# Kernel tuning notes

Measured on AMD Instinct MI355X. Metric: run time of the kernel, lower is better.

Reference implementation:

```python
import jax, jax.numpy as jnp
import numpy as np
import itertools

RANKS_HIGH = 15
SUITS_HIGH = 5
B, M = 16, 24
# Omaha unspool: choose 2 of 4 hole cards x choose 3 of 5 board cards -> 60 five-card combos
COMBOS = np.array([h + b for h in itertools.combinations(range(4), 2)
                   for b in itertools.combinations(range(4, 9), 3)], dtype=np.int32)  # [60, 5]


def setup_inputs() -> dict:
    key = jax.random.key(0)
    ks = list(jax.random.split(key, 20))
    f = lambda i, shape: jax.random.normal(ks[i], shape, jnp.float32) * 0.05
    ranks = jax.random.randint(ks[0], (B, M, 9), 2, RANKS_HIGH)  # card ranks 2..14
    suits = jax.random.randint(ks[1], (B, M, 9), 1, SUITS_HIGH)  # suits 1..4
    x = jnp.stack([ranks, suits], axis=-1).reshape(B, M, 18)     # alternating rank/suit
    ones16 = jnp.ones((16,), jnp.float32)
    zeros16 = jnp.zeros((16,), jnp.float32)
    return {
        "x": x,
        "suit_w": f(2, (16, 5, 1)), "suit_b": f(3, (16,)),
        "rank_w": f(4, (16, 5, 5)), "rank_b": f(5, (16,)),
        "bn_s_gamma": ones16, "bn_s_beta": zeros16, "bn_s_mean": zeros16, "bn_s_var": ones16,
        "bn_r_gamma": ones16, "bn_r_beta": zeros16, "bn_r_mean": zeros16, "bn_r_var": ones16,
        "w1": f(6, (32, 16)), "b1": f(7, (32,)),
        "w2": f(8, (32, 32)), "b2": f(9, (32,)),
        "wc": f(10, (7463, 512)), "bc": f(11, (7463,)),
        "wo1": f(12, (512, 15360)), "bo1": f(13, (512,)),
        "wo2": f(14, (256, 512)), "bo2": f(15, (256,)),
        "wo3": f(16, (127, 256)), "bo3": f(17, (127,)),
    }


def _bn(t, gamma, beta, mean, var, eps=1e-5):
    # eval-mode BatchNorm1d; channel axis is -2 (shape [..., 16, L])
    inv = gamma / jnp.sqrt(var + eps)
    return t * inv[:, None] + (beta - mean * inv)[:, None]


def _forward(x, suit_w, suit_b, bn_s_gamma, bn_s_beta, bn_s_mean, bn_s_var,
             rank_w, rank_b, bn_r_gamma, bn_r_beta, bn_r_mean, bn_r_var,
             w1, b1, w2, b2, wc, bc, wo1, bo1, wo2, bo2, wo3, bo3):
    b, m, _ = x.shape
    ranks = x[..., 0::2][..., COMBOS]  # [B,M,60,5]
    suits = x[..., 1::2][..., COMBOS]  # [B,M,60,5]
    hot_r = jax.nn.one_hot(ranks, RANKS_HIGH, dtype=jnp.float32)  # [B,M,60,5,15]
    hot_s = jax.nn.one_hot(suits, SUITS_HIGH, dtype=jnp.float32)  # [B,M,60,5,5]
    # suit conv: Conv1d(5,16,k=1) over the one-hot length; channels = 5 cards
    s = jnp.einsum('bmkcl,oc->bmkol', hot_s, suit_w[:, :, 0]) + suit_b[:, None]
    s = jax.nn.relu(_bn(s, bn_s_gamma, bn_s_beta, bn_s_mean, bn_s_var))  # [B,M,60,16,5]
    # rank conv: Conv1d(5,16,k=5) valid: length 15 -> 11
    n = b * m * 60
    r = jax.lax.conv_general_dilated(hot_r.reshape(n, 5, RANKS_HIGH), rank_w,
                                     window_strides=(1,), padding='VALID',
                                     dimension_numbers=('NCH', 'OIH', 'NCH'))
    r = r.reshape(b, m, 60, 16, 11) + rank_b[:, None]
    r = jax.nn.relu(_bn(r, bn_r_gamma, bn_r_beta, bn_r_mean, bn_r_var))  # [B,M,60,16,11]
    raw = jnp.concatenate([r, s], axis=-1)  # [B,M,60,16,16]
    # hand-class head: two hidden linears on last dim, then 512 -> 7463
    h = jax.nn.relu(raw @ w1.T + b1)        # [B,M,60,16,32]
    h = jax.nn.relu(h @ w2.T + b2)          # [B,M,60,16,32]
    logits = h.reshape(b, m, 60, 512) @ wc.T + bc  # [B,M,60,7463]
    best = jnp.min(jnp.argmax(jax.lax.stop_gradient(logits), axis=-1),
                   axis=-1, keepdims=True)  # [B,M,1] (lower class index = better hand)
    # raw-feature head: [B,M,60*16*16=15360] -> 512 -> 256 -> 127
    o = raw.reshape(b, m, 60 * 16 * 16)
    o = jax.nn.relu(o @ wo1.T + bo1)
    o = jax.nn.relu(o @ wo2.T + bo2)
    o = jax.nn.relu(o @ wo3.T + bo3)
    return jnp.concatenate([o, best.astype(o.dtype)], axis=-1)  # [B,M,128]


def reference(x, suit_w, suit_b, bn_s_gamma, bn_s_beta, bn_s_mean, bn_s_var,
              rank_w, rank_b, bn_r_gamma, bn_r_beta, bn_r_mean, bn_r_var,
              w1, b1, w2, b2, wc, bc, wo1, bo1, wo2, bo2, wo3, bo3):
    return _forward(x, suit_w, suit_b, bn_s_gamma, bn_s_beta, bn_s_mean, bn_s_var,
                    rank_w, rank_b, bn_r_gamma, bn_r_beta, bn_r_mean, bn_r_var,
                    w1, b1, w2, b2, wc, bc, wo1, bo1, wo2, bo2, wo3, bo3)
```

## Files before the change

kernel.cpp:

```cpp
#include <hip/hip_runtime.h>

#define NSAMP 384
#define NCOMBO 60
#define NROW 23040
#define KDIM 512
#define NCLS 7463
#define NCLSP 7680
#define NTILE_N 30
#define NTILE_M 180
#define O1_NZ 30
#define O1_KZ 512

typedef short s16x8 __attribute__((ext_vector_type(8)));
typedef short s16x4 __attribute__((ext_vector_type(4)));
typedef float f32x4 __attribute__((ext_vector_type(4)));

__device__ unsigned short g_wc_hi[NCLSP * KDIM];
__device__ unsigned short g_wc_lo[NCLSP * KDIM];
__device__ unsigned short g_h_hi[NROW * KDIM];
__device__ unsigned short g_h_lo[NROW * KDIM];
__device__ unsigned short g_rawbf[NROW * 256];
__device__ unsigned short g_wo1bf[512 * 15360];
__device__ float          g_pmax[NTILE_N * NROW];
__device__ int            g_pidx[NTILE_N * NROW];
__device__ float          g_part[O1_NZ * NSAMP * 512];

__device__ __forceinline__ float bf2f(unsigned short u){
  union { unsigned int i; float f; } v; v.i = ((unsigned int)u) << 16; return v.f;
}
__device__ __forceinline__ unsigned short f2bf(float f){
  union { float f; unsigned int i; } v; v.f = f;
  unsigned int u = v.i;
  unsigned int r = (u + 0x7FFFu + ((u >> 16) & 1u)) >> 16;
  return (unsigned short)r;
}
__device__ __forceinline__ void gload16(const void* g, void* l){
  __builtin_amdgcn_global_load_lds((const __attribute__((address_space(1))) void*)g,
                                   (__attribute__((address_space(3))) void*)l, 16, 0, 0);
}

__global__ __launch_bounds__(256) void k_prep(const float* __restrict__ wc,
                                              const float* __restrict__ wo1)
{
  int b = blockIdx.x;
  if (b < 3840){
    int idx = (b * 256 + threadIdx.x) * 4;
    float4 w = {0.f, 0.f, 0.f, 0.f};
    if (idx < NCLS * KDIM) w = *(const float4*)(wc + idx);
    s16x4 hi, lo;
    float wv[4] = {w.x, w.y, w.z, w.w};
    #pragma unroll
    for (int i = 0; i < 4; ++i){
      unsigned short h = f2bf(wv[i]);
      hi[i] = (short)h;
      lo[i] = (short)f2bf(wv[i] - bf2f(h));
    }
    *(s16x4*)(g_wc_hi + idx) = hi;
    *(s16x4*)(g_wc_lo + idx) = lo;
  } else {
    int idx = ((b - 3840) * 256 + threadIdx.x) * 4;
    float4 w = *(const float4*)(wo1 + idx);
    s16x4 v;
    v[0] = (short)f2bf(w.x); v[1] = (short)f2bf(w.y);
    v[2] = (short)f2bf(w.z); v[3] = (short)f2bf(w.w);
    *(s16x4*)(g_wo1bf + idx) = v;
  }
}

__global__ __launch_bounds__(256) void k_features(
    const int* __restrict__ x,
    const float* __restrict__ suit_w, const float* __restrict__ suit_b,
    const float* __restrict__ rank_w, const float* __restrict__ rank_b,
    const float* __restrict__ bns_g, const float* __restrict__ bns_b,
    const float* __restrict__ bns_m, const float* __restrict__ bns_v,
    const float* __restrict__ bnr_g, const float* __restrict__ bnr_b,
    const float* __restrict__ bnr_m, const float* __restrict__ bnr_v,
    const float* __restrict__ w1, const float* __restrict__ b1,
    const float* __restrict__ w2, const float* __restrict__ b2)
{
  __shared__ float raw_s[4][256];
  __shared__ float h1_s[4][512];
  const int tid  = threadIdx.x;
  const int lane = tid & 63;
  const int wv   = tid >> 6;
  const int combo = blockIdx.x * 4 + wv;
  const int s = combo / 60;
  const int k = combo % 60;
  const int hp = k / 10, bt = k % 10;
  const int HP0[6]  = {0,0,0,1,1,2}, HP1[6] = {1,2,3,2,3,3};
  const int BT0[10] = {4,4,4,4,4,4,5,5,5,6};
  const int BT1[10] = {5,5,5,6,6,7,6,6,7,7};
  const int BT2[10] = {6,7,8,7,8,8,7,8,8,8};
  int cards[5] = {HP0[hp], HP1[hp], BT0[bt], BT1[bt], BT2[bt]};
  const int* xp = x + s * 18;
  int rk[5], st[5];
  #pragma unroll
  for (int c = 0; c < 5; ++c){ rk[c] = xp[2*cards[c]]; st[c] = xp[2*cards[c] + 1]; }

  {
    s16x4 rv;
    #pragma unroll
    for (int i = 0; i < 4; ++i){
      int e = lane * 4 + i;
      int o = e >> 4, l = e & 15;
      float v;
      if (l < 11){
        float a = 0.f;
        #pragma unroll
        for (int c = 0; c < 5; ++c){
          int d = rk[c] - l;
          if (d >= 0 && d < 5) a += rank_w[o*25 + c*5 + d];
        }
        a += rank_b[o];
        float inv = bnr_g[o] / sqrtf(bnr_v[o] + 1e-5f);
        v = a * inv + (bnr_b[o] - bnr_m[o] * inv);
      } else {
        int j = l - 11;
        float a = suit_b[o];
        #pragma unroll
        for (int c = 0; c < 5; ++c) if (st[c] == j) a += suit_w[o*5 + c];
        float inv = bns_g[o] / sqrtf(bns_v[o] + 1e-5f);
        v = a * inv + (bns_b[o] - bns_m[o] * inv);
      }
      v = fmaxf(v, 0.f);
      raw_s[wv][e] = v;
      rv[i] = (short)f2bf(v);
    }
    *(s16x4*)(g_rawbf + (size_t)s * 15360 + k * 256 + lane * 4) = rv;
  }
  __syncthreads();
  #pragma unroll
  for (int i = 0; i < 8; ++i){
    int e = lane + 64 * i;
    int o = e >> 5, j = e & 31;
    float a = b1[j];
    #pragma unroll
    for (int l = 0; l < 16; ++l) a += raw_s[wv][o*16 + l] * w1[j*16 + l];
    h1_s[wv][e] = fmaxf(a, 0.f);
  }
  __syncthreads();
  {
    s16x8 hv, lv;
    #pragma unroll
    for (int i = 0; i < 8; ++i){
      int e = lane * 8 + i;
      int o = e >> 5, j = e & 31;
      float a = b2[j];
      #pragma unroll
      for (int l = 0; l < 32; ++l) a += h1_s[wv][o*32 + l] * w2[j*32 + l];
      a = fmaxf(a, 0.f);
      unsigned short h = f2bf(a);
      hv[i] = (short)h;
      lv[i] = (short)f2bf(a - bf2f(h));
    }
    *(s16x8*)(g_h_hi + (size_t)combo * 512 + lane * 8) = hv;
    *(s16x8*)(g_h_lo + (size_t)combo * 512 + lane * 8) = lv;
  }
}

__global__ __launch_bounds__(512, 4) void k_logits(const float* __restrict__ bc)
{
  __shared__ unsigned char lds[49152];
  const int tid  = threadIdx.x;
  const int lane = tid & 63;
  const int wv   = tid >> 6;
  const int wm   = wv >> 2, wn = wv & 3;
  const int blk  = blockIdx.x;
  const int nt   = blk / NTILE_M;
  const int mt   = blk % NTILE_M;
  const int m0 = mt * 128;
  const int n0 = nt * 256;

  f32x4 acc[4][4];
  #pragma unroll
  for (int i = 0; i < 4; ++i)
    #pragma unroll
    for (int j = 0; j < 4; ++j)
      acc[i][j] = (f32x4){0.f, 0.f, 0.f, 0.f};

  const int rS = wv * 16 + (lane >> 2);
  const int cS = (lane & 3) ^ ((lane >> 3) & 3);
  auto stage = [&](int buf, int t){
    const int p = t / 3, seg = t - p * 3;
    const int kc = p * 32;
    const unsigned short* As = (seg < 2) ? g_h_hi : g_h_lo;
    const unsigned short* Bs = (seg == 1) ? g_wc_lo : g_wc_hi;
    const unsigned base = buf * 24576 + wv * 1024;
    gload16(As + (size_t)(m0 + rS) * KDIM + kc + cS * 8, lds + base);
    gload16(Bs + (size_t)(n0 + rS) * KDIM + kc + cS * 8, lds + base + 8192);
    gload16(Bs + (size_t)(n0 + 128 + rS) * KDIM + kc + cS * 8, lds + base + 16384);
  };

  stage(0, 0);
  stage(1, 1);
  asm volatile("s_waitcnt vmcnt(3)" ::: "memory");
  __builtin_amdgcn_sched_barrier(0);
  __builtin_amdgcn_s_barrier();
  asm volatile("" ::: "memory");

  const int q = lane >> 4;
  #pragma unroll 1
  for (int t = 0; t < 48; ++t){
    const unsigned cb = (unsigned)(t & 1) * 24576;
    s16x8 af[4], bf[4];
    #pragma unroll
    for (int i = 0; i < 4; ++i){
      int row = wm * 64 + i * 16 + (lane & 15);
      af[i] = *(const s16x8*)(lds + cb + row * 64 + ((q ^ ((row >> 1) & 3)) << 4));
    }
    #pragma unroll
    for (int j = 0; j < 4; ++j){
      int row = wn * 64 + j * 16 + (lane & 15);
      bf[j] = *(const s16x8*)(lds + cb + 8192 + row * 64 + ((q ^ ((row >> 1) & 3)) << 4));
    }
    __builtin_amdgcn_s_setprio(1);
    #pragma unroll
    for (int i = 0; i < 4; ++i)
      #pragma unroll
      for (int j = 0; j < 4; ++j)
        acc[i][j] = __builtin_amdgcn_mfma_f32_16x16x32_bf16(af[i], bf[j], acc[i][j], 0, 0, 0);
    __builtin_amdgcn_s_setprio(0);
    __builtin_amdgcn_sched_barrier(0);
    __builtin_amdgcn_s_barrier();
    asm volatile("" ::: "memory");
    if (t + 2 < 48){
      stage(t & 1, t + 2);
      asm volatile("s_waitcnt vmcnt(3)" ::: "memory");
    } else {
      asm volatile("s_waitcnt vmcnt(0)" ::: "memory");
    }
    __builtin_amdgcn_sched_barrier(0);
    __builtin_amdgcn_s_barrier();
    asm volatile("" ::: "memory");
  }

  float* cmax = (float*)lds;
  int*   cidx = (int*)(lds + 2048);
  const int g = lane >> 4;
  #pragma unroll
  for (int i = 0; i < 4; ++i){
    #pragma unroll
    for (int r = 0; r < 4; ++r){
      float bv = -__builtin_inff(); int bi = 0x7FFFFFFF;
      #pragma unroll
      for (int j = 0; j < 4; ++j){
        int col = n0 + wn * 64 + j * 16 + (lane & 15);
        if (col < NCLS){
          float v = acc[i][j][r] + bc[col];
          if (v > bv){ bv = v; bi = col; }
        }
      }
      for (int s = 1; s < 16; s <<= 1){
        float ov = __shfl_xor(bv, s);
        int   oi = __shfl_xor(bi, s);
        if (ov > bv || (ov == bv && oi < bi)){ bv = ov; bi = oi; }
      }
      if ((lane & 15) == 0){
        int rloc = wm * 64 + i * 16 + g * 4 + r;
        cmax[rloc * 4 + wn] = bv;
        cidx[rloc * 4 + wn] = bi;
      }
    }
  }
  __syncthreads();
  if (tid < 128){
    float bv = cmax[tid * 4]; int bi = cidx[tid * 4];
    #pragma unroll
    for (int wq = 1; wq < 4; ++wq){
      float v = cmax[tid * 4 + wq]; int i1 = cidx[tid * 4 + wq];
      if (v > bv || (v == bv && i1 < bi)){ bv = v; bi = i1; }
    }
    size_t row = (size_t)(m0 + tid);
    g_pmax[(size_t)nt * NROW + row] = bv;
    g_pidx[(size_t)nt * NROW + row] = bi;
  }
}

__global__ __launch_bounds__(256) void k_o1(void)
{
  __shared__ unsigned char As[16384];
  __shared__ unsigned char Bs[16384];
  const int tid  = threadIdx.x;
  const int lane = tid & 63;
  const int wv   = tid >> 6;
  const int wr   = wv >> 1, wq = wv & 1;
  const int n0  = blockIdx.x * 128;
  const int m0  = blockIdx.y * 128;
  const int kc0 = blockIdx.z * O1_KZ;

  f32x4 acc[4][4];
  #pragma unroll
  for (int i = 0; i < 4; ++i)
    #pragma unroll
    for (int j = 0; j < 4; ++j)
      acc[i][j] = (f32x4){0.f, 0.f, 0.f, 0.f};

  const int rA = lane >> 3;
  const int c0 = lane & 7;
  for (int kk = 0; kk < O1_KZ; kk += 64){
    int kc = kc0 + kk;
    __syncthreads();
    #pragma unroll
    for (int it = 0; it < 4; ++it){
      int seg = wv * 4 + it;
      int r   = seg * 8 + rA;
      int cs  = c0 ^ (r & 7);
      gload16(g_rawbf + (size_t)(m0 + r) * 15360 + kc + cs * 8, As + seg * 1024);
      gload16(g_wo1bf + (size_t)(n0 + r) * 15360 + kc + cs * 8, Bs + seg * 1024);
    }
    __syncthreads();
    #pragma unroll
    for (int ks = 0; ks < 2; ++ks){
      int q = ks * 4 + (lane >> 4);
      s16x8 a[4];
      #pragma unroll
      for (int i = 0; i < 4; ++i){
        int row = wr * 64 + i * 16 + (lane & 15);
        a[i] = *(const s16x8*)(As + row * 128 + ((q ^ (row & 7)) * 16));
      }
      #pragma unroll
      for (int j = 0; j < 4; ++j){
        int col = wq * 64 + j * 16 + (lane & 15);
        s16x8 b = *(const s16x8*)(Bs + col * 128 + ((q ^ (col & 7)) * 16));
        #pragma unroll
        for (int i = 0; i < 4; ++i)
          acc[i][j] = __builtin_amdgcn_mfma_f32_16x16x32_bf16(a[i], b, acc[i][j], 0, 0, 0);
      }
    }
  }
  const int g = lane >> 4;
  #pragma unroll
  for (int i = 0; i < 4; ++i)
    #pragma unroll
    for (int j = 0; j < 4; ++j)
      #pragma unroll
      for (int r = 0; r < 4; ++r){
        int gm = m0 + wr * 64 + i * 16 + g * 4 + r;
        int gn = n0 + wq * 64 + j * 16 + (lane & 15);
        g_part[((size_t)blockIdx.z * NSAMP + gm) * 512 + gn] = acc[i][j][r];
      }
}

__global__ __launch_bounds__(256) void k_tail(
    const float* __restrict__ bo1, const float* __restrict__ wo2,
    const float* __restrict__ bo2, const float* __restrict__ wo3,
    const float* __restrict__ bo3, float* __restrict__ out)
{
  __shared__ float o1f[512];
  __shared__ float o2f[256];
  __shared__ int   bis[60];
  const int s = blockIdx.x;
  const int tid = threadIdx.x;
  if (tid < 60){
    size_t row = (size_t)s * 60 + tid;
    float bv = -__builtin_inff(); int bi = 0x7FFFFFFF;
    for (int qn = 0; qn < NTILE_N; ++qn){
      float v = g_pmax[(size_t)qn * NROW + row];
      int   i = g_pidx[(size_t)qn * NROW + row];
      if (v > bv || (v == bv && i < bi)){ bv = v; bi = i; }
    }
    bis[tid] = bi;
  }
  for (int j = tid; j < 512; j += 256){
    float a = bo1[j];
    for (int ks = 0; ks < O1_NZ; ++ks) a += g_part[((size_t)ks * NSAMP + s) * 512 + j];
    o1f[j] = fmaxf(a, 0.f);
  }
  __syncthreads();
  {
    float a = bo2[tid];
    const float* wr = wo2 + (size_t)tid * 512;
    for (int i = 0; i < 512; i += 4){
      float4 w4 = *(const float4*)(wr + i);
      a += o1f[i]*w4.x + o1f[i+1]*w4.y + o1f[i+2]*w4.z + o1f[i+3]*w4.w;
    }
    o2f[tid] = fmaxf(a, 0.f);
  }
  __syncthreads();
  if (tid < 127){
    float a = bo3[tid];
    const float* wr = wo3 + (size_t)tid * 256;
    for (int i = 0; i < 256; i += 4){
      float4 w4 = *(const float4*)(wr + i);
      a += o2f[i]*w4.x + o2f[i+1]*w4.y + o2f[i+2]*w4.z + o2f[i+3]*w4.w;
    }
    out[s * 128 + tid] = fmaxf(a, 0.f);
  }
  if (tid == 0){
    int m = bis[0];
    for (int i = 1; i < 60; ++i) m = min(m, bis[i]);
    out[s * 128 + 127] = (float)m;
  }
}

extern "C" void kernel_launch(void* const* d_in, const int* in_sizes, int n_in,
                              void* d_out, int out_size, void* d_ws, size_t ws_size,
                              hipStream_t stream)
{
  (void)d_ws; (void)ws_size; (void)in_sizes; (void)n_in; (void)out_size;
  const int*   x      = (const int*)  d_in[0];
  const float* suit_w = (const float*)d_in[1];
  const float* suit_b = (const float*)d_in[2];
  const float* rank_w = (const float*)d_in[3];
  const float* rank_b = (const float*)d_in[4];
  const float* bns_g  = (const float*)d_in[5];
  const float* bns_b  = (const float*)d_in[6];
  const float* bns_m  = (const float*)d_in[7];
  const float* bns_v  = (const float*)d_in[8];
  const float* bnr_g  = (const float*)d_in[9];
  const float* bnr_b  = (const float*)d_in[10];
  const float* bnr_m  = (const float*)d_in[11];
  const float* bnr_v  = (const float*)d_in[12];
  const float* w1     = (const float*)d_in[13];
  const float* b1     = (const float*)d_in[14];
  const float* w2     = (const float*)d_in[15];
  const float* b2     = (const float*)d_in[16];
  const float* wc     = (const float*)d_in[17];
  const float* bc     = (const float*)d_in[18];
  const float* wo1    = (const float*)d_in[19];
  const float* bo1    = (const float*)d_in[20];
  const float* wo2    = (const float*)d_in[21];
  const float* bo2    = (const float*)d_in[22];
  const float* wo3    = (const float*)d_in[23];
  const float* bo3    = (const float*)d_in[24];
  float* out = (float*)d_out;

  hipLaunchKernelGGL(k_prep, dim3(11520), dim3(256), 0, stream, wc, wo1);
  hipLaunchKernelGGL(k_features, dim3(5760), dim3(256), 0, stream, x,
                     suit_w, suit_b, rank_w, rank_b,
                     bns_g, bns_b, bns_m, bns_v, bnr_g, bnr_b, bnr_m, bnr_v,
                     w1, b1, w2, b2);
  hipLaunchKernelGGL(k_logits, dim3(NTILE_N * NTILE_M), dim3(512), 0, stream, bc);
  hipLaunchKernelGGL(k_o1, dim3(4, 3, O1_NZ), dim3(256), 0, stream);
  hipLaunchKernelGGL(k_tail, dim3(NSAMP), dim3(256), 0, stream,
                     bo1, wo2, bo2, wo3, bo3, out);
}
```

Measured before the change: 1.083 ms.

## Double the logits GEMM M tile and deepen to a four-stage LDS pipeline

The k_logits GEMM block tile grows from 128x256 to 256x256, so each warp accumulates 8x4 MFMA tiles and reuses its B fragments across two A halves. Global-to-LDS staging becomes a 4-buffer ring that prefetches three k-steps ahead, in 128KB of dynamic shared memory. The LDS layout drops the XOR swizzle for a chunk-major 16-row layout, and the argmax epilogue is widened to 256 rows. The aim is to cut the global traffic of re-reading Wc per M tile and to hide load latency better. The cost is one block per CU, higher register pressure, and possible LDS bank conflicts or a launch failure if the large dynamic LDS request is not allowed.

After: 1.158 ms. 1.07x slower.

```diff
diff --git a/kernel.cpp b/kernel.cpp
--- a/kernel.cpp
+++ b/kernel.cpp
@@ -7,7 +7,7 @@
 #define NCLS 7463
 #define NCLSP 7680
 #define NTILE_N 30
-#define NTILE_M 180
+#define NTILE_M 90
 #define O1_NZ 30
 #define O1_KZ 512
 
@@ -158,9 +158,9 @@
   }
 }
 
-__global__ __launch_bounds__(512, 4) void k_logits(const float* __restrict__ bc)
-{
-  __shared__ unsigned char lds[49152];
+__global__ __launch_bounds__(512, 2) void k_logits(const float* __restrict__ bc)
+{
+  extern __shared__ unsigned char lds[];
   const int tid  = threadIdx.x;
   const int lane = tid & 63;
   const int wv   = tid >> 6;
@@ -168,77 +168,87 @@
   const int blk  = blockIdx.x;
   const int nt   = blk / NTILE_M;
   const int mt   = blk % NTILE_M;
-  const int m0 = mt * 128;
+  const int m0 = mt * 256;
   const int n0 = nt * 256;
 
-  f32x4 acc[4][4];
-  #pragma unroll
-  for (int i = 0; i < 4; ++i)
+  f32x4 acc[8][4];
+  #pragma unroll
+  for (int i = 0; i < 8; ++i)
     #pragma unroll
     for (int j = 0; j < 4; ++j)
       acc[i][j] = (f32x4){0.f, 0.f, 0.f, 0.f};
 
-  const int rS = wv * 16 + (lane >> 2);
-  const int cS = (lane & 3) ^ ((lane >> 3) & 3);
-  auto stage = [&](int buf, int t){
-    const int p = t / 3, seg = t - p * 3;
+  const int srow = lane & 15;
+  const int schk = lane >> 4;
+
+  auto stage_one = [&](int t, int it){
+    const int p = t / 3, seg3 = t - p * 3;
     const int kc = p * 32;
-    const unsigned short* As = (seg < 2) ? g_h_hi : g_h_lo;
-    const unsigned short* Bs = (seg == 1) ? g_wc_lo : g_wc_hi;
-    const unsigned base = buf * 24576 + wv * 1024;
-    gload16(As + (size_t)(m0 + rS) * KDIM + kc + cS * 8, lds + base);
-    gload16(Bs + (size_t)(n0 + rS) * KDIM + kc + cS * 8, lds + base + 8192);
-    gload16(Bs + (size_t)(n0 + 128 + rS) * KDIM + kc + cS * 8, lds + base + 16384);
+    const unsigned short* As = (seg3 < 2) ? g_h_hi : g_h_lo;
+    const unsigned short* Bs = (seg3 == 1) ? g_wc_lo : g_wc_hi;
+    const int sg = it * 8 + wv;
+    const unsigned db = ((unsigned)(t & 3)) * 32768 + sg * 1024;
+    gload16(As + (size_t)(m0 + sg * 16 + srow) * KDIM + kc + schk * 8, lds + db);
+    gload16(Bs + (size_t)(n0 + sg * 16 + srow) * KDIM + kc + schk * 8, lds + db + 16384);
   };
 
-  stage(0, 0);
-  stage(1, 1);
-  asm volatile("s_waitcnt vmcnt(3)" ::: "memory");
+  #pragma unroll
+  for (int t = 0; t < 3; ++t){ stage_one(t, 0); stage_one(t, 1); }
+  asm volatile("s_waitcnt vmcnt(8)" ::: "memory");
   __builtin_amdgcn_sched_barrier(0);
   __builtin_amdgcn_s_barrier();
-  asm volatile("" ::: "memory");
-
-  const int q = lane >> 4;
+
+  const int rr = lane & 15;
+  const int qq = lane >> 4;
+  s16x8 af[4], bfr[4];
   #pragma unroll 1
   for (int t = 0; t < 48; ++t){
-    const unsigned cb = (unsigned)(t & 1) * 24576;
-    s16x8 af[4], bf[4];
-    #pragma unroll
-    for (int i = 0; i < 4; ++i){
-      int row = wm * 64 + i * 16 + (lane & 15);
-      af[i] = *(const s16x8*)(lds + cb + row * 64 + ((q ^ ((row >> 1) & 3)) << 4));
-    }
-    #pragma unroll
-    for (int j = 0; j < 4; ++j){
-      int row = wn * 64 + j * 16 + (lane & 15);
-      bf[j] = *(const s16x8*)(lds + cb + 8192 + row * 64 + ((q ^ ((row >> 1) & 3)) << 4));
-    }
+    const unsigned cb = ((unsigned)(t & 3)) * 32768;
+    const unsigned ab = cb + wm * 8192 + qq * 256 + rr * 16;
+    const unsigned bb = cb + 16384 + wn * 4096 + qq * 256 + rr * 16;
+    #pragma unroll
+    for (int j = 0; j < 4; ++j) bfr[j] = *(const s16x8*)(lds + bb + j * 1024);
+    #pragma unroll
+    for (int i = 0; i < 4; ++i) af[i] = *(const s16x8*)(lds + ab + i * 1024);
+    if (t < 45) stage_one(t + 3, 0);
+    __builtin_amdgcn_s_barrier();
+    asm volatile("s_waitcnt lgkmcnt(0)" ::: "memory");
+    __builtin_amdgcn_sched_barrier(0);
     __builtin_amdgcn_s_setprio(1);
     #pragma unroll
     for (int i = 0; i < 4; ++i)
       #pragma unroll
       for (int j = 0; j < 4; ++j)
-        acc[i][j] = __builtin_amdgcn_mfma_f32_16x16x32_bf16(af[i], bf[j], acc[i][j], 0, 0, 0);
+        acc[i][j] = __builtin_amdgcn_mfma_f32_16x16x32_bf16(af[i], bfr[j], acc[i][j], 0, 0, 0);
     __builtin_amdgcn_s_setprio(0);
     __builtin_amdgcn_sched_barrier(0);
     __builtin_amdgcn_s_barrier();
-    asm volatile("" ::: "memory");
-    if (t + 2 < 48){
-      stage(t & 1, t + 2);
-      asm volatile("s_waitcnt vmcnt(3)" ::: "memory");
-    } else {
-      asm volatile("s_waitcnt vmcnt(0)" ::: "memory");
-    }
+    #pragma unroll
+    for (int i = 0; i < 4; ++i) af[i] = *(const s16x8*)(lds + ab + (4 + i) * 1024);
+    if (t < 45) stage_one(t + 3, 1);
+    __builtin_amdgcn_s_barrier();
+    asm volatile("s_waitcnt lgkmcnt(0)" ::: "memory");
+    __builtin_amdgcn_sched_barrier(0);
+    __builtin_amdgcn_s_setprio(1);
+    #pragma unroll
+    for (int i = 0; i < 4; ++i)
+      #pragma unroll
+      for (int j = 0; j < 4; ++j)
+        acc[4 + i][j] = __builtin_amdgcn_mfma_f32_16x16x32_bf16(af[i], bfr[j], acc[4 + i][j], 0, 0, 0);
+    __builtin_amdgcn_s_setprio(0);
+    __builtin_amdgcn_sched_barrier(0);
+    if (t < 45)       asm volatile("s_waitcnt vmcnt(8)" ::: "memory");
+    else if (t == 45) asm volatile("s_waitcnt vmcnt(4)" ::: "memory");
+    else if (t == 46) asm volatile("s_waitcnt vmcnt(0)" ::: "memory");
     __builtin_amdgcn_sched_barrier(0);
     __builtin_amdgcn_s_barrier();
-    asm volatile("" ::: "memory");
   }
 
   float* cmax = (float*)lds;
-  int*   cidx = (int*)(lds + 2048);
+  int*   cidx = (int*)(lds + 4096);
   const int g = lane >> 4;
   #pragma unroll
-  for (int i = 0; i < 4; ++i){
+  for (int i = 0; i < 8; ++i){
     #pragma unroll
     for (int r = 0; r < 4; ++r){
       float bv = -__builtin_inff(); int bi = 0x7FFFFFFF;
@@ -256,14 +266,14 @@
         if (ov > bv || (ov == bv && oi < bi)){ bv = ov; bi = oi; }
       }
       if ((lane & 15) == 0){
-        int rloc = wm * 64 + i * 16 + g * 4 + r;
+        int rloc = wm * 128 + i * 16 + g * 4 + r;
         cmax[rloc * 4 + wn] = bv;
         cidx[rloc * 4 + wn] = bi;
       }
     }
   }
   __syncthreads();
-  if (tid < 128){
+  if (tid < 256){
     float bv = cmax[tid * 4]; int bi = cidx[tid * 4];
     #pragma unroll
     for (int wq = 1; wq < 4; ++wq){
@@ -430,7 +440,7 @@
                      suit_w, suit_b, rank_w, rank_b,
                      bns_g, bns_b, bns_m, bns_v, bnr_g, bnr_b, bnr_m, bnr_v,
                      w1, b1, w2, b2);
-  hipLaunchKernelGGL(k_logits, dim3(NTILE_N * NTILE_M), dim3(512), 0, stream, bc);
+  hipLaunchKernelGGL(k_logits, dim3(NTILE_N * NTILE_M), dim3(512), 131072, stream, bc);
   hipLaunchKernelGGL(k_o1, dim3(4, 3, O1_NZ), dim3(256), 0, stream);
   hipLaunchKernelGGL(k_tail, dim3(NSAMP), dim3(256), 0, stream,
                      bo1, wo2, bo2, wo3, bo3, out);
```

## Retile logits GEMM to 256x64 blocks with A fragments streamed from global

Applied to the files above, without the earlier changes.

The hand-class logits GEMM moves from 128x256 tiles with 512 threads to 256x64 tiles with 256 threads. Each wave now loads its A (hidden-activation) MFMA fragments straight from global memory into registers, double-buffered across k-steps, and only the small B (weight) slice goes through a double-buffered LDS buffer. The per-block argmax no longer needs a cross-wave LDS reduction, because each wave owns the full 64-column slice of its rows. In exchange there are four times as many column tiles, so the A operand is re-read from L2 far more often, and the partial-argmax buffer and its downstream reduction grow to 120 tiles per row.

After: 1.652 ms. 52.6% more time.

```diff
diff --git a/kernel.cpp b/kernel.cpp
--- a/kernel.cpp
+++ b/kernel.cpp
@@ -6,8 +6,8 @@
 #define KDIM 512
 #define NCLS 7463
 #define NCLSP 7680
-#define NTILE_N 30
-#define NTILE_M 180
+#define NTILE_N 120
+#define NTILE_M 90
 #define O1_NZ 30
 #define O1_KZ 512
 
@@ -158,18 +158,19 @@
   }
 }
 
-__global__ __launch_bounds__(512, 4) void k_logits(const float* __restrict__ bc)
-{
-  __shared__ unsigned char lds[49152];
+__global__ __launch_bounds__(256, 3) void k_logits(const float* __restrict__ bc)
+{
+  __shared__ unsigned char Blds[10240];
   const int tid  = threadIdx.x;
   const int lane = tid & 63;
   const int wv   = tid >> 6;
-  const int wm   = wv >> 2, wn = wv & 3;
+  const int cc   = lane & 15;
+  const int qq   = lane >> 4;
   const int blk  = blockIdx.x;
-  const int nt   = blk / NTILE_M;
-  const int mt   = blk % NTILE_M;
-  const int m0 = mt * 128;
-  const int n0 = nt * 256;
+  const int mt   = blk / NTILE_N;
+  const int nt   = blk % NTILE_N;
+  const int m0 = mt * 256;
+  const int n0 = nt * 64;
 
   f32x4 acc[4][4];
   #pragma unroll
@@ -178,65 +179,68 @@
     for (int j = 0; j < 4; ++j)
       acc[i][j] = (f32x4){0.f, 0.f, 0.f, 0.f};
 
-  const int rS = wv * 16 + (lane >> 2);
-  const int cS = (lane & 3) ^ ((lane >> 3) & 3);
-  auto stage = [&](int buf, int t){
-    const int p = t / 3, seg = t - p * 3;
-    const int kc = p * 32;
-    const unsigned short* As = (seg < 2) ? g_h_hi : g_h_lo;
-    const unsigned short* Bs = (seg == 1) ? g_wc_lo : g_wc_hi;
-    const unsigned base = buf * 24576 + wv * 1024;
-    gload16(As + (size_t)(m0 + rS) * KDIM + kc + cS * 8, lds + base);
-    gload16(Bs + (size_t)(n0 + rS) * KDIM + kc + cS * 8, lds + base + 8192);
-    gload16(Bs + (size_t)(n0 + 128 + rS) * KDIM + kc + cS * 8, lds + base + 16384);
-  };
-
-  stage(0, 0);
-  stage(1, 1);
-  asm volatile("s_waitcnt vmcnt(3)" ::: "memory");
-  __builtin_amdgcn_sched_barrier(0);
-  __builtin_amdgcn_s_barrier();
-  asm volatile("" ::: "memory");
-
-  const int q = lane >> 4;
-  #pragma unroll 1
-  for (int t = 0; t < 48; ++t){
-    const unsigned cb = (unsigned)(t & 1) * 24576;
-    s16x8 af[4], bf[4];
-    #pragma unroll
-    for (int i = 0; i < 4; ++i){
-      int row = wm * 64 + i * 16 + (lane & 15);
-      af[i] = *(const s16x8*)(lds + cb + row * 64 + ((q ^ ((row >> 1) & 3)) << 4));
-    }
-    #pragma unroll
-    for (int j = 0; j < 4; ++j){
-      int row = wn * 64 + j * 16 + (lane & 15);
-      bf[j] = *(const s16x8*)(lds + cb + 8192 + row * 64 + ((q ^ ((row >> 1) & 3)) << 4));
-    }
+  const int arow = m0 + wv * 64 + cc;
+  const int bcol = n0 + wv * 16 + cc;
+  const unsigned bwoff = (wv * 16 + cc) * 80 + qq * 16;
+
+  s16x8 aA[4], aB[4];
+  s16x8 brA, brB;
+  s16x8 bFr[4];
+
+  {
+    brA = *(const s16x8*)(g_wc_hi + (size_t)bcol * KDIM + 0 + qq * 8);
+    brB = *(const s16x8*)(g_wc_lo + (size_t)bcol * KDIM + 0 + qq * 8);
+    #pragma unroll
+    for (int i = 0; i < 4; ++i)
+      aA[i] = *(const s16x8*)(g_h_hi + (size_t)(arow + i * 16) * KDIM + 0 + qq * 8);
+    asm volatile("s_waitcnt vmcnt(5)" ::: "memory");
+    *(s16x8*)(Blds + bwoff) = brA;
+    asm volatile("s_waitcnt lgkmcnt(0)" ::: "memory");
+    __builtin_amdgcn_sched_barrier(0);
+    __builtin_amdgcn_s_barrier();
+  }
+
+  auto tile_body = [&](s16x8 (&CUR)[4], s16x8 (&NXT)[4], s16x8& brC, s16x8& brN, int t){
+    const unsigned bb = (unsigned)(t & 1) * 5120;
+    #pragma unroll
+    for (int j = 0; j < 4; ++j)
+      bFr[j] = *(const s16x8*)(Blds + bb + (j * 16 + cc) * 80 + qq * 16);
+    if (t + 2 < 48){
+      int t2 = t + 2, p2 = t2 / 3, sg2 = t2 - p2 * 3;
+      const unsigned short* Bg = (sg2 == 1) ? g_wc_lo : g_wc_hi;
+      brN = *(const s16x8*)(Bg + (size_t)bcol * KDIM + p2 * 32 + qq * 8);
+    }
+    if (t + 1 < 48){
+      int t1 = t + 1, p1 = t1 / 3, sg1 = t1 - p1 * 3;
+      const unsigned short* Ag = (sg1 < 2) ? g_h_hi : g_h_lo;
+      #pragma unroll
+      for (int i = 0; i < 4; ++i)
+        NXT[i] = *(const s16x8*)(Ag + (size_t)(arow + i * 16) * KDIM + p1 * 32 + qq * 8);
+    }
+    if (t < 46)       asm volatile("s_waitcnt vmcnt(5)" ::: "memory");
+    else if (t == 46) asm volatile("s_waitcnt vmcnt(4)" ::: "memory");
+    else              asm volatile("s_waitcnt vmcnt(0)" ::: "memory");
+    if (t + 1 < 48)
+      *(s16x8*)(Blds + (unsigned)((t + 1) & 1) * 5120 + bwoff) = brC;
+    asm volatile("s_waitcnt lgkmcnt(0)" ::: "memory");
+    __builtin_amdgcn_sched_barrier(0);
     __builtin_amdgcn_s_setprio(1);
     #pragma unroll
     for (int i = 0; i < 4; ++i)
       #pragma unroll
       for (int j = 0; j < 4; ++j)
-        acc[i][j] = __builtin_amdgcn_mfma_f32_16x16x32_bf16(af[i], bf[j], acc[i][j], 0, 0, 0);
+        acc[i][j] = __builtin_amdgcn_mfma_f32_16x16x32_bf16(CUR[i], bFr[j], acc[i][j], 0, 0, 0);
     __builtin_amdgcn_s_setprio(0);
     __builtin_amdgcn_sched_barrier(0);
     __builtin_amdgcn_s_barrier();
-    asm volatile("" ::: "memory");
-    if (t + 2 < 48){
-      stage(t & 1, t + 2);
-      asm volatile("s_waitcnt vmcnt(3)" ::: "memory");
-    } else {
-      asm volatile("s_waitcnt vmcnt(0)" ::: "memory");
-    }
-    __builtin_amdgcn_sched_barrier(0);
-    __builtin_amdgcn_s_barrier();
-    asm volatile("" ::: "memory");
-  }
-
-  float* cmax = (float*)lds;
-  int*   cidx = (int*)(lds + 2048);
-  const int g = lane >> 4;
+  };
+
+  #pragma unroll 1
+  for (int tp = 0; tp < 24; ++tp){
+    tile_body(aA, aB, brB, brA, tp * 2);
+    tile_body(aB, aA, brA, brB, tp * 2 + 1);
+  }
+
   #pragma unroll
   for (int i = 0; i < 4; ++i){
     #pragma unroll
@@ -244,7 +248,7 @@
       float bv = -__builtin_inff(); int bi = 0x7FFFFFFF;
       #pragma unroll
       for (int j = 0; j < 4; ++j){
-        int col = n0 + wn * 64 + j * 16 + (lane & 15);
+        int col = n0 + j * 16 + cc;
         if (col < NCLS){
           float v = acc[i][j][r] + bc[col];
           if (v > bv){ bv = v; bi = col; }
@@ -255,24 +259,13 @@
         int   oi = __shfl_xor(bi, s);
         if (ov > bv || (ov == bv && oi < bi)){ bv = ov; bi = oi; }
       }
-      if ((lane & 15) == 0){
-        int rloc = wm * 64 + i * 16 + g * 4 + r;
-        cmax[rloc * 4 + wn] = bv;
-        cidx[rloc * 4 + wn] = bi;
-      }
-    }
-  }
-  __syncthreads();
-  if (tid < 128){
-    float bv = cmax[tid * 4]; int bi = cidx[tid * 4];
-    #pragma unroll
-    for (int wq = 1; wq < 4; ++wq){
-      float v = cmax[tid * 4 + wq]; int i1 = cidx[tid * 4 + wq];
-      if (v > bv || (v == bv && i1 < bi)){ bv = v; bi = i1; }
-    }
-    size_t row = (size_t)(m0 + tid);
-    g_pmax[(size_t)nt * NROW + row] = bv;
-    g_pidx[(size_t)nt * NROW + row] = bi;
+      if (cc == 0){
+        int rloc = wv * 64 + i * 16 + qq * 4 + r;
+        size_t row = (size_t)(m0 + rloc);
+        g_pmax[(size_t)nt * NROW + row] = bv;
+        g_pidx[(size_t)nt * NROW + row] = bi;
+      }
+    }
   }
 }
 
@@ -430,7 +423,7 @@
                      suit_w, suit_b, rank_w, rank_b,
                      bns_g, bns_b, bns_m, bns_v, bnr_g, bnr_b, bnr_m, bnr_v,
                      w1, b1, w2, b2);
-  hipLaunchKernelGGL(k_logits, dim3(NTILE_N * NTILE_M), dim3(512), 0, stream, bc);
+  hipLaunchKernelGGL(k_logits, dim3(NTILE_M * NTILE_N), dim3(256), 0, stream, bc);
   hipLaunchKernelGGL(k_o1, dim3(4, 3, O1_NZ), dim3(256), 0, stream);
   hipLaunchKernelGGL(k_tail, dim3(NSAMP), dim3(256), 0, stream,
                      bo1, wo2, bo2, wo3, bo3, out);
```

## Replace split-bf16 logits GEMM with fp16 GEMM plus top-2 exact rescoring

Applied to the files above, without the earlier changes.

Drops the three-pass hi/lo bf16 split for the 23040x7463x512 logits GEMM and uses a single fp16 MFMA pass, cutting MFMA work and operand traffic to about a third. To keep the argmax exact, each tile now keeps a top-2 candidate list. When the winner's margin is small, the tail kernel rescored near-tie candidates in double precision from fp32 weights and fp32 activations. The GEMM is also retiled to 128x128 tiles with 256 threads, a 64-wide K step, and an XCD-aware block mapping. In exchange it stores an extra fp32 copy of the activations and has a rare serial rescoring path in k_tail.

Measured after the change: 2.366 ms. 2.19x slower.

```diff
diff --git a/kernel.cpp b/kernel.cpp
--- a/kernel.cpp
+++ b/kernel.cpp
@@ -6,7 +6,7 @@
 #define KDIM 512
 #define NCLS 7463
 #define NCLSP 7680
-#define NTILE_N 30
+#define NTILE_N 60
 #define NTILE_M 180
 #define O1_NZ 30
 #define O1_KZ 512
@@ -14,15 +14,17 @@
 typedef short s16x8 __attribute__((ext_vector_type(8)));
 typedef short s16x4 __attribute__((ext_vector_type(4)));
 typedef float f32x4 __attribute__((ext_vector_type(4)));
-
-__device__ unsigned short g_wc_hi[NCLSP * KDIM];
-__device__ unsigned short g_wc_lo[NCLSP * KDIM];
-__device__ unsigned short g_h_hi[NROW * KDIM];
-__device__ unsigned short g_h_lo[NROW * KDIM];
+typedef _Float16 f16x8 __attribute__((ext_vector_type(8)));
+
+__device__ unsigned short g_wc_f16[NCLSP * KDIM];
+__device__ unsigned short g_h_f16[NROW * KDIM];
+__device__ float          g_h_f32[NROW * KDIM];
 __device__ unsigned short g_rawbf[NROW * 256];
 __device__ unsigned short g_wo1bf[512 * 15360];
-__device__ float          g_pmax[NTILE_N * NROW];
-__device__ int            g_pidx[NTILE_N * NROW];
+__device__ float          g_p1v[NTILE_N * NROW];
+__device__ int            g_p1i[NTILE_N * NROW];
+__device__ float          g_p2v[NTILE_N * NROW];
+__device__ int            g_p2i[NTILE_N * NROW];
 __device__ float          g_part[O1_NZ * NSAMP * 512];
 
 __device__ __forceinline__ float bf2f(unsigned short u){
@@ -34,9 +36,17 @@
   unsigned int r = (u + 0x7FFFu + ((u >> 16) & 1u)) >> 16;
   return (unsigned short)r;
 }
+__device__ __forceinline__ unsigned short f2h(float f){
+  union { _Float16 h; unsigned short s; } cv; cv.h = (_Float16)f; return cv.s;
+}
 __device__ __forceinline__ void gload16(const void* g, void* l){
   __builtin_amdgcn_global_load_lds((const __attribute__((address_space(1))) void*)g,
                                    (__attribute__((address_space(3))) void*)l, 16, 0, 0);
+}
+__device__ __forceinline__ void top2_merge(float& v1, int& i1, float& v2, int& i2,
+                                           float wv, int wi){
+  if (wv > v1 || (wv == v1 && wi < i1)){ v2 = v1; i2 = i1; v1 = wv; i1 = wi; }
+  else if (wv > v2 || (wv == v2 && wi < i2)){ v2 = wv; i2 = wi; }
 }
 
 __global__ __launch_bounds__(256) void k_prep(const float* __restrict__ wc,
@@ -47,16 +57,9 @@
     int idx = (b * 256 + threadIdx.x) * 4;
     float4 w = {0.f, 0.f, 0.f, 0.f};
     if (idx < NCLS * KDIM) w = *(const float4*)(wc + idx);
-    s16x4 hi, lo;
-    float wv[4] = {w.x, w.y, w.z, w.w};
-    #pragma unroll
-    for (int i = 0; i < 4; ++i){
-      unsigned short h = f2bf(wv[i]);
-      hi[i] = (short)h;
-      lo[i] = (short)f2bf(wv[i] - bf2f(h));
-    }
-    *(s16x4*)(g_wc_hi + idx) = hi;
-    *(s16x4*)(g_wc_lo + idx) = lo;
+    ushort4 h;
+    h.x = f2h(w.x); h.y = f2h(w.y); h.z = f2h(w.z); h.w = f2h(w.w);
+    *(ushort4*)(g_wc_f16 + idx) = h;
   } else {
     int idx = ((b - 3840) * 256 + threadIdx.x) * 4;
     float4 w = *(const float4*)(wo1 + idx);
@@ -140,7 +143,8 @@
   }
   __syncthreads();
   {
-    s16x8 hv, lv;
+    unsigned short hv[8];
+    float hf[8];
     #pragma unroll
     for (int i = 0; i < 8; ++i){
       int e = lane * 8 + i;
@@ -149,27 +153,32 @@
       #pragma unroll
       for (int l = 0; l < 32; ++l) a += h1_s[wv][o*32 + l] * w2[j*32 + l];
       a = fmaxf(a, 0.f);
-      unsigned short h = f2bf(a);
-      hv[i] = (short)h;
-      lv[i] = (short)f2bf(a - bf2f(h));
-    }
-    *(s16x8*)(g_h_hi + (size_t)combo * 512 + lane * 8) = hv;
-    *(s16x8*)(g_h_lo + (size_t)combo * 512 + lane * 8) = lv;
-  }
-}
-
-__global__ __launch_bounds__(512, 4) void k_logits(const float* __restrict__ bc)
-{
-  __shared__ unsigned char lds[49152];
+      hv[i] = f2h(a);
+      hf[i] = a;
+    }
+    *(ushort4*)(g_h_f16 + (size_t)combo * 512 + lane * 8)     = *(ushort4*)&hv[0];
+    *(ushort4*)(g_h_f16 + (size_t)combo * 512 + lane * 8 + 4) = *(ushort4*)&hv[4];
+    *(float4*)(g_h_f32 + (size_t)combo * 512 + lane * 8)     = *(float4*)&hf[0];
+    *(float4*)(g_h_f32 + (size_t)combo * 512 + lane * 8 + 4) = *(float4*)&hf[4];
+  }
+}
+
+__global__ __launch_bounds__(256, 2) void k_logits(const float* __restrict__ bc)
+{
+  __shared__ unsigned char lds[65536];
   const int tid  = threadIdx.x;
   const int lane = tid & 63;
   const int wv   = tid >> 6;
-  const int wm   = wv >> 2, wn = wv & 3;
-  const int blk  = blockIdx.x;
-  const int nt   = blk / NTILE_M;
-  const int mt   = blk % NTILE_M;
+  const int wr   = wv >> 1, wq = wv & 1;
+  const int flat  = blockIdx.x;
+  const int xcd   = flat & 7;
+  const int seq   = flat >> 3;
+  const int group = xcd >> 1;
+  const int par   = xcd & 1;
+  const int mt    = (seq / 15) * 2 + par;
+  const int nt    = group * 15 + (seq % 15);
   const int m0 = mt * 128;
-  const int n0 = nt * 256;
+  const int n0 = nt * 128;
 
   f32x4 acc[4][4];
   #pragma unroll
@@ -178,101 +187,92 @@
     for (int j = 0; j < 4; ++j)
       acc[i][j] = (f32x4){0.f, 0.f, 0.f, 0.f};
 
-  const int rS = wv * 16 + (lane >> 2);
-  const int cS = (lane & 3) ^ ((lane >> 3) & 3);
-  auto stage = [&](int buf, int t){
-    const int p = t / 3, seg = t - p * 3;
-    const int kc = p * 32;
-    const unsigned short* As = (seg < 2) ? g_h_hi : g_h_lo;
-    const unsigned short* Bs = (seg == 1) ? g_wc_lo : g_wc_hi;
-    const unsigned base = buf * 24576 + wv * 1024;
-    gload16(As + (size_t)(m0 + rS) * KDIM + kc + cS * 8, lds + base);
-    gload16(Bs + (size_t)(n0 + rS) * KDIM + kc + cS * 8, lds + base + 8192);
-    gload16(Bs + (size_t)(n0 + 128 + rS) * KDIM + kc + cS * 8, lds + base + 16384);
+  const int srow8 = tid >> 3;
+  const int sc0   = tid & 7;
+  auto stage = [&](int b, int kc){
+    const unsigned base = (unsigned)b * 32768;
+    #pragma unroll
+    for (int it = 0; it < 4; ++it){
+      int r  = it * 32 + srow8;
+      int cs = sc0 ^ (r & 7);
+      unsigned lb = base + it * 4096 + wv * 1024;
+      gload16(g_h_f16  + (size_t)(m0 + r) * KDIM + kc + cs * 8, lds + lb);
+      gload16(g_wc_f16 + (size_t)(n0 + r) * KDIM + kc + cs * 8, lds + lb + 16384);
+    }
   };
 
+  const int cc = lane & 15;
+  const int qq = lane >> 4;
+  int buf = 0;
   stage(0, 0);
-  stage(1, 1);
-  asm volatile("s_waitcnt vmcnt(3)" ::: "memory");
-  __builtin_amdgcn_sched_barrier(0);
-  __builtin_amdgcn_s_barrier();
-  asm volatile("" ::: "memory");
-
-  const int q = lane >> 4;
-  #pragma unroll 1
-  for (int t = 0; t < 48; ++t){
-    const unsigned cb = (unsigned)(t & 1) * 24576;
-    s16x8 af[4], bf[4];
-    #pragma unroll
-    for (int i = 0; i < 4; ++i){
-      int row = wm * 64 + i * 16 + (lane & 15);
-      af[i] = *(const s16x8*)(lds + cb + row * 64 + ((q ^ ((row >> 1) & 3)) << 4));
-    }
-    #pragma unroll
-    for (int j = 0; j < 4; ++j){
-      int row = wn * 64 + j * 16 + (lane & 15);
-      bf[j] = *(const s16x8*)(lds + cb + 8192 + row * 64 + ((q ^ ((row >> 1) & 3)) << 4));
-    }
-    __builtin_amdgcn_s_setprio(1);
-    #pragma unroll
-    for (int i = 0; i < 4; ++i)
-      #pragma unroll
-      for (int j = 0; j < 4; ++j)
-        acc[i][j] = __builtin_amdgcn_mfma_f32_16x16x32_bf16(af[i], bf[j], acc[i][j], 0, 0, 0);
-    __builtin_amdgcn_s_setprio(0);
-    __builtin_amdgcn_sched_barrier(0);
-    __builtin_amdgcn_s_barrier();
-    asm volatile("" ::: "memory");
-    if (t + 2 < 48){
-      stage(t & 1, t + 2);
-      asm volatile("s_waitcnt vmcnt(3)" ::: "memory");
-    } else {
-      asm volatile("s_waitcnt vmcnt(0)" ::: "memory");
-    }
-    __builtin_amdgcn_sched_barrier(0);
-    __builtin_amdgcn_s_barrier();
-    asm volatile("" ::: "memory");
-  }
-
-  float* cmax = (float*)lds;
-  int*   cidx = (int*)(lds + 2048);
-  const int g = lane >> 4;
+  __syncthreads();
+  for (int t = 0; t < 8; ++t){
+    if (t < 7) stage(buf ^ 1, (t + 1) * 64);
+    const unsigned base = (unsigned)buf * 32768;
+    #pragma unroll
+    for (int ks = 0; ks < 2; ++ks){
+      int q = ks * 4 + qq;
+      f16x8 a[4];
+      #pragma unroll
+      for (int i = 0; i < 4; ++i){
+        int row = wr * 64 + i * 16 + cc;
+        a[i] = *(const f16x8*)(lds + base + row * 128 + ((q ^ (row & 7)) * 16));
+      }
+      #pragma unroll
+      for (int j = 0; j < 4; ++j){
+        int col = wq * 64 + j * 16 + cc;
+        f16x8 b = *(const f16x8*)(lds + base + 16384 + col * 128 + ((q ^ (col & 7)) * 16));
+        #pragma unroll
+        for (int i = 0; i < 4; ++i)
+          acc[i][j] = __builtin_amdgcn_mfma_f32_16x16x32_f16(a[i], b, acc[i][j], 0, 0, 0);
+      }
+    }
+    __syncthreads();
+    buf ^= 1;
+  }
+
+  float* cm1 = (float*)lds;
+  int*   ci1 = (int*)(lds + 1024);
+  float* cm2 = (float*)(lds + 2048);
+  int*   ci2 = (int*)(lds + 3072);
   #pragma unroll
   for (int i = 0; i < 4; ++i){
     #pragma unroll
     for (int r = 0; r < 4; ++r){
-      float bv = -__builtin_inff(); int bi = 0x7FFFFFFF;
+      float v1 = -__builtin_inff(); int i1 = 0x7FFFFFFF;
+      float v2 = -__builtin_inff(); int i2 = 0x7FFFFFFF;
       #pragma unroll
       for (int j = 0; j < 4; ++j){
-        int col = n0 + wn * 64 + j * 16 + (lane & 15);
+        int col = n0 + wq * 64 + j * 16 + cc;
         if (col < NCLS){
           float v = acc[i][j][r] + bc[col];
-          if (v > bv){ bv = v; bi = col; }
+          top2_merge(v1, i1, v2, i2, v, col);
         }
       }
       for (int s = 1; s < 16; s <<= 1){
-        float ov = __shfl_xor(bv, s);
-        int   oi = __shfl_xor(bi, s);
-        if (ov > bv || (ov == bv && oi < bi)){ bv = ov; bi = oi; }
-      }
-      if ((lane & 15) == 0){
-        int rloc = wm * 64 + i * 16 + g * 4 + r;
-        cmax[rloc * 4 + wn] = bv;
-        cidx[rloc * 4 + wn] = bi;
+        float ov1 = __shfl_xor(v1, s); int oi1 = __shfl_xor(i1, s);
+        float ov2 = __shfl_xor(v2, s); int oi2 = __shfl_xor(i2, s);
+        top2_merge(v1, i1, v2, i2, ov1, oi1);
+        top2_merge(v1, i1, v2, i2, ov2, oi2);
+      }
+      if (cc == 0){
+        int rloc = wr * 64 + i * 16 + qq * 4 + r;
+        cm1[rloc * 2 + wq] = v1; ci1[rloc * 2 + wq] = i1;
+        cm2[rloc * 2 + wq] = v2; ci2[rloc * 2 + wq] = i2;
       }
     }
   }
   __syncthreads();
   if (tid < 128){
-    float bv = cmax[tid * 4]; int bi = cidx[tid * 4];
-    #pragma unroll
-    for (int wq = 1; wq < 4; ++wq){
-      float v = cmax[tid * 4 + wq]; int i1 = cidx[tid * 4 + wq];
-      if (v > bv || (v == bv && i1 < bi)){ bv = v; bi = i1; }
-    }
+    float v1 = cm1[tid * 2]; int i1 = ci1[tid * 2];
+    float v2 = cm2[tid * 2]; int i2 = ci2[tid * 2];
+    top2_merge(v1, i1, v2, i2, cm1[tid * 2 + 1], ci1[tid * 2 + 1]);
+    top2_merge(v1, i1, v2, i2, cm2[tid * 2 + 1], ci2[tid * 2 + 1]);
     size_t row = (size_t)(m0 + tid);
-    g_pmax[(size_t)nt * NROW + row] = bv;
-    g_pidx[(size_t)nt * NROW + row] = bi;
+    g_p1v[(size_t)nt * NROW + row] = v1;
+    g_p1i[(size_t)nt * NROW + row] = i1;
+    g_p2v[(size_t)nt * NROW + row] = v2;
+    g_p2i[(size_t)nt * NROW + row] = i2;
   }
 }
 
@@ -342,6 +342,7 @@
 }
 
 __global__ __launch_bounds__(256) void k_tail(
+    const float* __restrict__ wc, const float* __restrict__ bc,
     const float* __restrict__ bo1, const float* __restrict__ wo2,
     const float* __restrict__ bo2, const float* __restrict__ wo3,
     const float* __restrict__ bo3, float* __restrict__ out)
@@ -353,13 +354,42 @@
   const int tid = threadIdx.x;
   if (tid < 60){
     size_t row = (size_t)s * 60 + tid;
-    float bv = -__builtin_inff(); int bi = 0x7FFFFFFF;
-    for (int qn = 0; qn < NTILE_N; ++qn){
-      float v = g_pmax[(size_t)qn * NROW + row];
-      int   i = g_pidx[(size_t)qn * NROW + row];
-      if (v > bv || (v == bv && i < bi)){ bv = v; bi = i; }
-    }
-    bis[tid] = bi;
+    float v1 = -__builtin_inff(); int i1 = 0x7FFFFFFF;
+    float v2 = -__builtin_inff(); int i2 = 0x7FFFFFFF;
+    for (int q = 0; q < NTILE_N; ++q){
+      top2_merge(v1, i1, v2, i2, g_p1v[(size_t)q * NROW + row], g_p1i[(size_t)q * NROW + row]);
+      top2_merge(v1, i1, v2, i2, g_p2v[(size_t)q * NROW + row], g_p2i[(size_t)q * NROW + row]);
+    }
+    int best = i1;
+    float delta = fmaxf(1e-3f, 0.02f * fabsf(v1));
+    if (v1 - v2 <= delta){
+      float thr = v1 - delta;
+      int cand[8]; int cnt = 0;
+      for (int q = 0; q < NTILE_N && cnt < 8; ++q){
+        float a = g_p1v[(size_t)q * NROW + row];
+        if (a >= thr) cand[cnt++] = g_p1i[(size_t)q * NROW + row];
+        if (cnt < 8){
+          float b2v = g_p2v[(size_t)q * NROW + row];
+          if (b2v >= thr) cand[cnt++] = g_p2i[(size_t)q * NROW + row];
+        }
+      }
+      const float* hp = g_h_f32 + row * (size_t)KDIM;
+      double bv = -1e300; int bi = 0x7FFFFFFF;
+      for (int e = 0; e < cnt; ++e){
+        int c = cand[e];
+        const float* wp = wc + (size_t)c * KDIM;
+        double d = (double)bc[c];
+        for (int k2 = 0; k2 < KDIM; k2 += 4){
+          float4 hv = *(const float4*)(hp + k2);
+          float4 wv4 = *(const float4*)(wp + k2);
+          d += (double)hv.x * wv4.x + (double)hv.y * wv4.y
+             + (double)hv.z * wv4.z + (double)hv.w * wv4.w;
+        }
+        if (d > bv || (d == bv && c < bi)){ bv = d; bi = c; }
+      }
+      best = bi;
+    }
+    bis[tid] = best;
   }
   for (int j = tid; j < 512; j += 256){
     float a = bo1[j];
@@ -430,8 +460,8 @@
                      suit_w, suit_b, rank_w, rank_b,
                      bns_g, bns_b, bns_m, bns_v, bnr_g, bnr_b, bnr_m, bnr_v,
                      w1, b1, w2, b2);
-  hipLaunchKernelGGL(k_logits, dim3(NTILE_N * NTILE_M), dim3(512), 0, stream, bc);
+  hipLaunchKernelGGL(k_logits, dim3(NTILE_N * NTILE_M), dim3(256), 0, stream, bc);
   hipLaunchKernelGGL(k_o1, dim3(4, 3, O1_NZ), dim3(256), 0, stream);
   hipLaunchKernelGGL(k_tail, dim3(NSAMP), dim3(256), 0, stream,
-                     bo1, wo2, bo2, wo3, bo3, out);
-}
+                     wc, bc, bo1, wo2, bo2, wo3, bo3, out);
+}
```
